# Kernel tuning notes

Hardware: AMD Instinct MI355X
Metric: run time of the kernel (lower is better)

Reference implementation:

```python
import jax, jax.numpy as jnp
import numpy as np

MIN_POS = 1e-6
EPS = 1e-20
B, S, F_IN, E, H = 2, 1024, 768, 768, 12
DH = E // H   # nnmf in_features per head (64)
FH = E // H   # nnmf out_features per head (hidden_features=embed_dim default)
N_NNMF_ITERS = 3
N_ALPHA_ITERS = 3


def l1norm(x, axis=-1):
    # F.normalize(x, p=1, dim=axis, eps=1e-20) for non-negative x
    return x / jnp.maximum(jnp.sum(jnp.abs(x), axis=axis, keepdims=True), EPS)


def setup_inputs() -> dict:
    key = jax.random.key(0)
    k = jax.random.split(key, 6)
    return {
        "x": jax.random.normal(k[0], (B, S, F_IN), jnp.float32),
        "embed_w": jax.random.normal(k[1], (E, F_IN), jnp.float32) * 0.02,
        "embed_b": jnp.zeros((E,), jnp.float32),
        "nnmf_w": jax.random.uniform(k[2], (FH, DH), jnp.float32),  # non-negative NMF dictionary
        "out_w": jax.random.normal(k[3], (F_IN, E), jnp.float32) * 0.02,
        "out_b": jnp.zeros((F_IN,), jnp.float32),
    }


def reference(x, embed_w, embed_b, nnmf_w, out_w, out_b):
    # normalize NMF weight rows (p=1 over in_features), as nnmf_layer.normalize_weights
    W = nnmf_w / jnp.maximum(jnp.sum(nnmf_w, axis=1, keepdims=True), EPS)  # [FH, DH]

    # embed + clamp positive, split heads
    xe = jnp.clip(x @ embed_w.T + embed_b, MIN_POS)            # [B,S,E]
    xe = xe.reshape(B, S, H, DH)                                # [B,S,H,DH]

    # NNMFDense: prepared_input = l1-normalized input (normalize_input_dim=-1)
    inp = l1norm(xe)                                            # [B,S,H,DH]
    h = l1norm(jnp.ones((B, S, H, FH), x.dtype))                # init hidden
    rec = inp
    for _ in range(N_NNMF_ITERS):
        rec = l1norm(jnp.clip(h @ W, MIN_POS))                  # reconstruction [B,S,H,DH]
        h = l1norm(jnp.clip(h * ((inp / rec) @ W.T), MIN_POS))  # multiplicative update

    # normalize_h (p=1, dim=-1)
    h = l1norm(h)                                               # [B,S,H,FH] -> 'bohf'

    # alpha dynamics fixed point
    alpha = jnp.ones((B, H, S, S), x.dtype)                     # 'bhoi'
    h_rec_input = rec * inp                                     # [B,S,H,DH]
    for _ in range(N_ALPHA_ITERS):
        h_mixed = jnp.einsum('bohf,bhoi->bihf', h, alpha)       # [B,S,H,FH]
        arec_inv = 1.0 / (h_mixed @ W + EPS)                    # _reconstruct -> [B,S,H,DH]
        alpha = alpha * jnp.einsum('bohf,bihf->bhoi', h_rec_input, arec_inv)

    out = jnp.einsum('bohf,bhoi->bihf', h, alpha)               # [B,S,H,FH]
    out = out.reshape(B, S, E)                                  # flatten heads
    return out @ out_w.T + out_b                                # out_project
```

## Files before the change

kernel.cpp:

```cpp
#include <hip/hip_runtime.h>

#define B_  2
#define S_  1024
#define FIN 768
#define E_  768
#define H_  12
#define DH  64

typedef unsigned int uint;
typedef unsigned short ushort;
typedef __attribute__((ext_vector_type(8))) short short8;
typedef __attribute__((ext_vector_type(4))) float floatx4;

__device__ __forceinline__ ushort f2bf(float f) {
    uint u = __float_as_uint(f);
    return (ushort)((u + 0x7fffu + ((u >> 16) & 1u)) >> 16);
}

__device__ __forceinline__ uint4 pack8(const ushort* p) {
    uint4 r;
    r.x = (uint)p[0] | ((uint)p[1] << 16);
    r.y = (uint)p[2] | ((uint)p[3] << 16);
    r.z = (uint)p[4] | ((uint)p[5] << 16);
    r.w = (uint)p[6] | ((uint)p[7] << 16);
    return r;
}

__device__ __forceinline__ void split8v(float4 a, float4 b, short8& hi, short8& lo) {
    float v[8] = {a.x, a.y, a.z, a.w, b.x, b.y, b.z, b.w};
    ushort h[8], l[8];
#pragma unroll
    for (int j = 0; j < 8; ++j) {
        h[j] = f2bf(v[j]);
        l[j] = f2bf(v[j] - __uint_as_float(((uint)h[j]) << 16));
    }
    uint4 H = pack8(h), L = pack8(l);
    hi = *(short8*)&H;
    lo = *(short8*)&L;
}

__global__ __launch_bounds__(256) void k_embed_prep(const float* __restrict__ xs,
                                                    const float* __restrict__ ew,
                                                    const float* __restrict__ eb,
                                                    const float* __restrict__ nw,
                                                    float* __restrict__ Wn,
                                                    float* __restrict__ WnT,
                                                    float* __restrict__ r1inv,
                                                    float* __restrict__ inp) {
    __shared__ __align__(16) unsigned char smem[28160];
    const int tid = threadIdx.x;
    const int bid = blockIdx.x;

    if (bid >= 768) {
        float* Wl = (float*)smem;
        const int f = tid >> 2, q = tid & 3;
        float v[16];
        float s = 0.f;
#pragma unroll
        for (int i = 0; i < 16; ++i) { v[i] = nw[f * 64 + q * 16 + i]; s += v[i]; }
        s += __shfl_xor(s, 1, 64);
        s += __shfl_xor(s, 2, 64);
        const float inv = 1.f / fmaxf(s, 1e-20f);
#pragma unroll
        for (int i = 0; i < 16; ++i) {
            float w = v[i] * inv;
            Wn[f * 64 + q * 16 + i] = w;
            WnT[(q * 16 + i) * 64 + f] = w;
            Wl[f * 65 + q * 16 + i] = w;
        }
        __syncthreads();
        if (tid < 64) {
            float cs = 0.f;
            for (int ff = 0; ff < 64; ++ff) cs += Wl[ff * 65 + tid];
            float t = fmaxf(cs * (1.f / 64.f), 1e-6f);
            float S = t;
#pragma unroll
            for (int m = 1; m < 64; m <<= 1) S += __shfl_xor(S, m, 64);
            S = fmaxf(S, 1e-20f);
            r1inv[tid] = S / t;
        }
        return;
    }

    const int head = bid % 12;
    const int tok0 = (bid / 12) * 32;
    ushort* As_hi = (ushort*)smem;
    ushort* As_lo = As_hi + 32 * 72;
    ushort* Bs_hi = As_lo + 32 * 72;
    ushort* Bs_lo = Bs_hi + 64 * 72;
    float*  RS    = (float*)(Bs_lo + 64 * 72);

    const int wv = tid >> 6, lane = tid & 63;
    const int mbase = (wv >> 1) * 16;
    const int nbase = (wv & 1) * 32;
    const int lm = lane & 15, lq = lane >> 4;

    floatx4 accA[2], accB[2];
    accA[0] = (floatx4)0.f; accA[1] = (floatx4)0.f;
    accB[0] = (floatx4)0.f; accB[1] = (floatx4)0.f;

    const int arow = tid >> 3, akc = (tid & 7) * 8;
    const int brow = tid >> 2, bkq = (tid & 3) * 16;
    const float* xrow = xs + (size_t)(tok0 + arow) * FIN + akc;
    const float* wrg  = ew + (size_t)(head * 64 + brow) * FIN + bkq;

    float4 pa[2], pb[4];
#pragma unroll
    for (int c = 0; c < 2; ++c) pa[c] = *(const float4*)(xrow + c * 4);
#pragma unroll
    for (int c = 0; c < 4; ++c) pb[c] = *(const float4*)(wrg + c * 4);

    for (int kb = 0; kb < FIN; kb += 64) {
        __syncthreads();
        {
            short8 Ah, Al, B0h, B0l, B1h, B1l;
            split8v(pa[0], pa[1], Ah, Al);
            split8v(pb[0], pb[1], B0h, B0l);
            split8v(pb[2], pb[3], B1h, B1l);
            const int aoff = arow * 72 + akc;
            *(short8*)&As_hi[aoff] = Ah;
            *(short8*)&As_lo[aoff] = Al;
            const int boff = brow * 72 + bkq;
            *(short8*)&Bs_hi[boff]     = B0h;
            *(short8*)&Bs_hi[boff + 8] = B1h;
            *(short8*)&Bs_lo[boff]     = B0l;
            *(short8*)&Bs_lo[boff + 8] = B1l;
        }
        __syncthreads();
        if (kb + 64 < FIN) {
#pragma unroll
            for (int c = 0; c < 2; ++c) pa[c] = *(const float4*)(xrow + kb + 64 + c * 4);
#pragma unroll
            for (int c = 0; c < 4; ++c) pb[c] = *(const float4*)(wrg + kb + 64 + c * 4);
        }
#pragma unroll
        for (int ch = 0; ch < 2; ++ch) {
            const int ko = ch * 32 + lq * 8;
            short8 ah = *(const short8*)&As_hi[(mbase + lm) * 72 + ko];
            short8 al = *(const short8*)&As_lo[(mbase + lm) * 72 + ko];
#pragma unroll
            for (int ti = 0; ti < 2; ++ti) {
                short8 bh = *(const short8*)&Bs_hi[(nbase + ti * 16 + lm) * 72 + ko];
                short8 bl = *(const short8*)&Bs_lo[(nbase + ti * 16 + lm) * 72 + ko];
                accA[ti] = __builtin_amdgcn_mfma_f32_16x16x32_bf16(ah, bh, accA[ti], 0, 0, 0);
                accB[ti] = __builtin_amdgcn_mfma_f32_16x16x32_bf16(al, bh, accB[ti], 0, 0, 0);
                accB[ti] = __builtin_amdgcn_mfma_f32_16x16x32_bf16(ah, bl, accB[ti], 0, 0, 0);
            }
        }
    }

    const float b0 = eb[head * 64 + nbase + lm];
    const float b1 = eb[head * 64 + nbase + 16 + lm];
    float xe[2][4];
    float rs[4];
#pragma unroll
    for (int r = 0; r < 4; ++r) {
        float e0 = fmaxf((accA[0][r] + accB[0][r]) + b0, 1e-6f);
        float e1 = fmaxf((accA[1][r] + accB[1][r]) + b1, 1e-6f);
        xe[0][r] = e0; xe[1][r] = e1;
        float p = e0 + e1;
        p += __shfl_xor(p, 1, 64);
        p += __shfl_xor(p, 2, 64);
        p += __shfl_xor(p, 4, 64);
        p += __shfl_xor(p, 8, 64);
        rs[r] = p;
    }
    if (lm == 0) {
#pragma unroll
        for (int r = 0; r < 4; ++r)
            RS[(wv & 1) * 32 + mbase + lq * 4 + r] = rs[r];
    }
    __syncthreads();
    const size_t obase = ((size_t)((tok0 >> 10) * 12 + head) * 1024 + (tok0 & 1023));
#pragma unroll
    for (int r = 0; r < 4; ++r) {
        const int m = mbase + lq * 4 + r;
        const float inv = 1.f / fmaxf(RS[m] + RS[32 + m], 1e-20f);
        float* op = inp + (obase + m) * 64;
        op[nbase + lm]      = xe[0][r] * inv;
        op[nbase + 16 + lm] = xe[1][r] * inv;
    }
}

__device__ __forceinline__ void mfma_matvec(const float srcC[4][4], float* T,
                                            int lm, int lq,
                                            const ushort* WH, const ushort* WL,
                                            floatx4 out[4]) {
    __builtin_amdgcn_wave_barrier();
#pragma unroll
    for (int nt = 0; nt < 4; ++nt)
#pragma unroll
        for (int r = 0; r < 4; ++r)
            T[(lq * 4 + r) * 68 + nt * 16 + lm] = srcC[nt][r];
    __builtin_amdgcn_wave_barrier();
    float4 a00 = *(const float4*)&T[lm * 68 + lq * 8];
    float4 a01 = *(const float4*)&T[lm * 68 + lq * 8 + 4];
    float4 a10 = *(const float4*)&T[lm * 68 + 32 + lq * 8];
    float4 a11 = *(const float4*)&T[lm * 68 + 32 + lq * 8 + 4];
    __builtin_amdgcn_wave_barrier();
    short8 A0h, A0l, A1h, A1l;
    split8v(a00, a01, A0h, A0l);
    split8v(a10, a11, A1h, A1l);
#pragma unroll
    for (int nt = 0; nt < 4; ++nt) {
        const int row = (nt * 16 + lm) * 72;
        short8 b0h = *(const short8*)&WH[row + lq * 8];
        short8 b0l = *(const short8*)&WL[row + lq * 8];
        short8 b1h = *(const short8*)&WH[row + 32 + lq * 8];
        short8 b1l = *(const short8*)&WL[row + 32 + lq * 8];
        floatx4 acc0 = (floatx4)0.f, acc1 = (floatx4)0.f;
        acc0 = __builtin_amdgcn_mfma_f32_16x16x32_bf16(A0h, b0h, acc0, 0, 0, 0);
        acc0 = __builtin_amdgcn_mfma_f32_16x16x32_bf16(A0l, b0h, acc0, 0, 0, 0);
        acc0 = __builtin_amdgcn_mfma_f32_16x16x32_bf16(A0h, b0l, acc0, 0, 0, 0);
        acc1 = __builtin_amdgcn_mfma_f32_16x16x32_bf16(A1h, b1h, acc1, 0, 0, 0);
        acc1 = __builtin_amdgcn_mfma_f32_16x16x32_bf16(A1l, b1h, acc1, 0, 0, 0);
        acc1 = __builtin_amdgcn_mfma_f32_16x16x32_bf16(A1h, b1l, acc1, 0, 0, 0);
        out[nt] = acc0 + acc1;
    }
}

__global__ __launch_bounds__(256) void k_nnmf(const float* __restrict__ inp,
                                              const float* __restrict__ Wn,
                                              const float* __restrict__ WnT,
                                              const float* __restrict__ r1inv,
                                              float* __restrict__ hout,
                                              float* __restrict__ hriout,
                                              float* __restrict__ mp0) {
    __shared__ ushort WtH[64 * 72], WtL[64 * 72];
    __shared__ ushort WwH[64 * 72], WwL[64 * 72];
    __shared__ float Tb[4][16 * 68];
    __shared__ float pbuf[256];
    const int tid = threadIdx.x, wv = tid >> 6, lane = tid & 63;
    const int lm = lane & 15, lq = lane >> 4;
    float* T = Tb[wv];
    const int rowbase = blockIdx.x * 64 + wv * 16;

    {
        const int row = tid >> 2, kq = (tid & 3) * 16;
        short8 h0, l0, h1, l1;
        split8v(*(const float4*)(WnT + row * 64 + kq), *(const float4*)(WnT + row * 64 + kq + 4), h0, l0);
        split8v(*(const float4*)(WnT + row * 64 + kq + 8), *(const float4*)(WnT + row * 64 + kq + 12), h1, l1);
        *(short8*)&WtH[row * 72 + kq] = h0; *(short8*)&WtH[row * 72 + kq + 8] = h1;
        *(short8*)&WtL[row * 72 + kq] = l0; *(short8*)&WtL[row * 72 + kq + 8] = l1;
        split8v(*(const float4*)(Wn + row * 64 + kq), *(const float4*)(Wn + row * 64 + kq + 4), h0, l0);
        split8v(*(const float4*)(Wn + row * 64 + kq + 8), *(const float4*)(Wn + row * 64 + kq + 12), h1, l1);
        *(short8*)&WwH[row * 72 + kq] = h0; *(short8*)&WwH[row * 72 + kq + 8] = h1;
        *(short8*)&WwL[row * 72 + kq] = l0; *(short8*)&WwL[row * 72 + kq + 8] = l1;
    }

    float inpC[4][4];
#pragma unroll
    for (int nt = 0; nt < 4; ++nt)
#pragma unroll
        for (int r = 0; r < 4; ++r)
            inpC[nt][r] = inp[(size_t)(rowbase + lq * 4 + r) * 64 + nt * 16 + lm];
    float r1c[4];
#pragma unroll
    for (int nt = 0; nt < 4; ++nt) r1c[nt] = r1inv[nt * 16 + lm];
    __syncthreads();

    float hC[4][4], recC[4][4];
    {
        float qC[4][4];
#pragma unroll
        for (int nt = 0; nt < 4; ++nt)
#pragma unroll
            for (int r = 0; r < 4; ++r) qC[nt][r] = inpC[nt][r] * r1c[nt];
        floatx4 u[4];
        mfma_matvec(qC, T, lm, lq, WwH, WwL, u);
#pragma unroll
        for (int nt = 0; nt < 4; ++nt)
#pragma unroll
            for (int r = 0; r < 4; ++r)
                hC[nt][r] = fmaxf(u[nt][r] * (1.f / 64.f), 1e-6f);
#pragma unroll
        for (int r = 0; r < 4; ++r) {
            float s = (hC[0][r] + hC[1][r]) + (hC[2][r] + hC[3][r]);
            s += __shfl_xor(s, 1, 64); s += __shfl_xor(s, 2, 64);
            s += __shfl_xor(s, 4, 64); s += __shfl_xor(s, 8, 64);
            const float inv = __builtin_amdgcn_rcpf(fmaxf(s, 1e-20f));
#pragma unroll
            for (int nt = 0; nt < 4; ++nt) hC[nt][r] *= inv;
        }
    }
#pragma unroll 1
    for (int it = 0; it < 2; ++it) {
        floatx4 t[4];
        mfma_matvec(hC, T, lm, lq, WtH, WtL, t);
        float tC[4][4], qC[4][4];
#pragma unroll
        for (int nt = 0; nt < 4; ++nt)
#pragma unroll
            for (int r = 0; r < 4; ++r) tC[nt][r] = fmaxf(t[nt][r], 1e-6f);
#pragma unroll
        for (int r = 0; r < 4; ++r) {
            float s = (tC[0][r] + tC[1][r]) + (tC[2][r] + tC[3][r]);
            s += __shfl_xor(s, 1, 64); s += __shfl_xor(s, 2, 64);
            s += __shfl_xor(s, 4, 64); s += __shfl_xor(s, 8, 64);
            s = fmaxf(s, 1e-20f);
            const float invS = __builtin_amdgcn_rcpf(s);
#pragma unroll
            for (int nt = 0; nt < 4; ++nt) {
                recC[nt][r] = tC[nt][r] * invS;
                qC[nt][r] = inpC[nt][r] * s * __builtin_amdgcn_rcpf(tC[nt][r]);
            }
        }
        floatx4 u[4];
        mfma_matvec(qC, T, lm, lq, WwH, WwL, u);
#pragma unroll
        for (int nt = 0; nt < 4; ++nt)
#pragma unroll
            for (int r = 0; r < 4; ++r)
                hC[nt][r] = fmaxf(hC[nt][r] * u[nt][r], 1e-6f);
#pragma unroll
        for (int r = 0; r < 4; ++r) {
            float s = (hC[0][r] + hC[1][r]) + (hC[2][r] + hC[3][r]);
            s += __shfl_xor(s, 1, 64); s += __shfl_xor(s, 2, 64);
            s += __shfl_xor(s, 4, 64); s += __shfl_xor(s, 8, 64);
            const float inv = __builtin_amdgcn_rcpf(fmaxf(s, 1e-20f));
#pragma unroll
            for (int nt = 0; nt < 4; ++nt) hC[nt][r] *= inv;
        }
    }
#pragma unroll
    for (int r = 0; r < 4; ++r) {
        float s = (hC[0][r] + hC[1][r]) + (hC[2][r] + hC[3][r]);
        s += __shfl_xor(s, 1, 64); s += __shfl_xor(s, 2, 64);
        s += __shfl_xor(s, 4, 64); s += __shfl_xor(s, 8, 64);
        const float inv = __builtin_amdgcn_rcpf(fmaxf(s, 1e-20f));
#pragma unroll
        for (int nt = 0; nt < 4; ++nt) hC[nt][r] *= inv;
    }

#pragma unroll
    for (int nt = 0; nt < 4; ++nt)
#pragma unroll
        for (int r = 0; r < 4; ++r) {
            const size_t o = (size_t)(rowbase + lq * 4 + r) * 64 + nt * 16 + lm;
            hout[o] = hC[nt][r];
            hriout[o] = recC[nt][r] * inpC[nt][r];
        }

    float hs[4];
#pragma unroll
    for (int nt = 0; nt < 4; ++nt) {
        float s = (hC[nt][0] + hC[nt][1]) + (hC[nt][2] + hC[nt][3]);
        s += __shfl_xor(s, 16, 64);
        s += __shfl_xor(s, 32, 64);
        hs[nt] = s;
    }
    pbuf[wv * 64 + lq * 16 + lm] = hs[lq];
    __syncthreads();
    if (tid < 64) {
        float tot = (pbuf[tid] + pbuf[64 + tid]) + (pbuf[128 + tid] + pbuf[192 + tid]);
        mp0[(size_t)blockIdx.x * 64 + tid] = tot;
    }
}

__global__ __launch_bounds__(256) void k_alpha_step(const float* __restrict__ hin,
                                                    const float* __restrict__ hri,
                                                    const float* __restrict__ Wn,
                                                    const float* __restrict__ mp_in,
                                                    float* __restrict__ mp_out,
                                                    float* __restrict__ c,
                                                    int it) {
    __shared__ float mred[4][64];
    __shared__ float mv[64];
    __shared__ float vv[64];
    __shared__ float cl[64];
    const int tid = threadIdx.x;
    const int bh = blockIdx.x >> 4;
    const int chunk = blockIdx.x & 15;
    const size_t rowbase = (size_t)bh * 1024 + chunk * 64;

    {
        int f = tid & 63, p = tid >> 6;
        float s = 0.f;
#pragma unroll
        for (int pp = 0; pp < 4; ++pp)
            s += mp_in[((size_t)bh * 16 + p * 4 + pp) * 64 + f];
        mred[p][f] = s;
    }
    __syncthreads();
    if (tid < 64)
        mv[tid] = (mred[0][tid] + mred[1][tid]) + (mred[2][tid] + mred[3][tid]);
    __syncthreads();
    {
        int d = tid & 63, qq = tid >> 6;
        float r = 0.f;
#pragma unroll
        for (int ff = 0; ff < 16; ++ff)
            r = fmaf(mv[qq * 16 + ff], Wn[(size_t)(qq * 16 + ff) * 64 + d], r);
        mred[qq][d] = r;
    }
    __syncthreads();
    if (tid < 64)
        vv[tid] = 1.f / (((mred[0][tid] + mred[1][tid]) + (mred[2][tid] + mred[3][tid])) + 1e-20f);
    __syncthreads();
    {
        int o = tid >> 2, dq = tid & 3;
        const float* rp = hri + (rowbase + o) * 64 + dq * 16;
        float dot = 0.f;
#pragma unroll
        for (int t4 = 0; t4 < 16; t4 += 4) {
            float4 r4 = *(const float4*)(rp + t4);
            dot = fmaf(r4.x, vv[dq * 16 + t4 + 0], dot);
            dot = fmaf(r4.y, vv[dq * 16 + t4 + 1], dot);
            dot = fmaf(r4.z, vv[dq * 16 + t4 + 2], dot);
            dot = fmaf(r4.w, vv[dq * 16 + t4 + 3], dot);
        }
        dot += __shfl_xor(dot, 1, 64);
        dot += __shfl_xor(dot, 2, 64);
        float cn = dot;
        if (it >= 2) cn *= c[rowbase + o];
        if (dq == 0) { c[rowbase + o] = cn; cl[o] = cn; }
    }
    __syncthreads();
    {
        const int f4 = (tid & 15) * 4, ogr = tid >> 4;
        float4 a = make_float4(0.f, 0.f, 0.f, 0.f);
#pragma unroll
        for (int oi = 0; oi < 4; ++oi) {
            int o = ogr * 4 + oi;
            float4 h4 = *(const float4*)(hin + (rowbase + o) * 64 + f4);
            float cv = cl[o];
            a.x = fmaf(h4.x, cv, a.x); a.y = fmaf(h4.y, cv, a.y);
            a.z = fmaf(h4.z, cv, a.z); a.w = fmaf(h4.w, cv, a.w);
        }
        a.x += __shfl_xor(a.x, 16, 64); a.y += __shfl_xor(a.y, 16, 64);
        a.z += __shfl_xor(a.z, 16, 64); a.w += __shfl_xor(a.w, 16, 64);
        a.x += __shfl_xor(a.x, 32, 64); a.y += __shfl_xor(a.y, 32, 64);
        a.z += __shfl_xor(a.z, 32, 64); a.w += __shfl_xor(a.w, 32, 64);
        const int w = tid >> 6;
        if ((tid & 63) < 16) *(float4*)&mred[w][(tid & 15) * 4] = a;
    }
    __syncthreads();
    if (tid < 64) {
        float s = (mred[0][tid] + mred[1][tid]) + (mred[2][tid] + mred[3][tid]);
        mp_out[((size_t)bh * 16 + chunk) * 64 + tid] = s;
    }
}

__global__ __launch_bounds__(256) void k_projbcast(const float* __restrict__ mp3,
                                                   const float* __restrict__ ow,
                                                   const float* __restrict__ ob,
                                                   float* __restrict__ out) {
    __shared__ float Ml[768];
    __shared__ float ps[4][64];
    __shared__ float yseg[64];
    const int tid = threadIdx.x;
    const int b = blockIdx.x / 192;
    const int rem = blockIdx.x - b * 192;
    const int jt = rem >> 4, rg = rem & 15;
    for (int i = tid; i < 768; i += 256) {
        const int hh = i >> 6, f = i & 63;
        const float* src = mp3 + ((size_t)(b * 12 + hh) * 16) * 64 + f;
        float s = 0.f;
#pragma unroll
        for (int cc = 0; cc < 16; ++cc) s += src[cc * 64];
        Ml[i] = s;
    }
    __syncthreads();
    const int jj = tid & 63, part = tid >> 6;
    const int j = jt * 64 + jj;
    const float* row = ow + (size_t)j * 768 + part * 192;
    float acc = 0.f;
    for (int t = 0; t < 192; t += 4) {
        float4 w4 = *(const float4*)(row + t);
        acc = fmaf(w4.x, Ml[part * 192 + t + 0], acc);
        acc = fmaf(w4.y, Ml[part * 192 + t + 1], acc);
        acc = fmaf(w4.z, Ml[part * 192 + t + 2], acc);
        acc = fmaf(w4.w, Ml[part * 192 + t + 3], acc);
    }
    ps[part][jj] = acc;
    __syncthreads();
    if (tid < 64)
        yseg[tid] = ps[0][tid] + ps[1][tid] + ps[2][tid] + ps[3][tid] + ob[jt * 64 + tid];
    __syncthreads();
    const int r0 = tid >> 2, c4 = (tid & 3) * 16;
    float4 v4[4];
#pragma unroll
    for (int q = 0; q < 4; ++q) v4[q] = *(const float4*)&yseg[c4 + q * 4];
    float* dst = out + ((size_t)(b * 1024 + rg * 64 + r0)) * 768 + jt * 64 + c4;
#pragma unroll
    for (int q = 0; q < 4; ++q) *(float4*)(dst + q * 4) = v4[q];
}

extern "C" void kernel_launch(void* const* d_in, const int* in_sizes, int n_in,
                              void* d_out, int out_size, void* d_ws, size_t ws_size,
                              hipStream_t stream) {
    const float* xs = (const float*)d_in[0];
    const float* ew = (const float*)d_in[1];
    const float* eb = (const float*)d_in[2];
    const float* nw = (const float*)d_in[3];
    const float* ow = (const float*)d_in[4];
    const float* ob = (const float*)d_in[5];
    float* out = (float*)d_out;

    float* ws    = (float*)d_ws;
    float* inp   = ws;
    float* h     = ws + 1572864;
    float* hri   = ws + 3145728;
    float* Wn    = ws + 4718592;
    float* WnT   = ws + 4722688;
    float* r1inv = ws + 4726784;
    float* mp0   = ws + 4727040;
    float* mp1   = ws + 4751616;
    float* mp2   = ws + 4776192;
    float* c     = ws + 4800768;

    k_embed_prep<<<769, 256, 0, stream>>>(xs, ew, eb, nw, Wn, WnT, r1inv, inp);
    k_nnmf<<<384, 256, 0, stream>>>(inp, Wn, WnT, r1inv, h, hri, mp0);
    k_alpha_step<<<384, 256, 0, stream>>>(h, hri, Wn, mp0, mp1, c, 1);
    k_alpha_step<<<384, 256, 0, stream>>>(h, hri, Wn, mp1, mp2, c, 2);
    k_alpha_step<<<384, 256, 0, stream>>>(h, hri, Wn, mp2, mp1, c, 3);
    k_projbcast<<<384, 256, 0, stream>>>(mp1, ow, ob, out);
}
```

Measured before the change: 133.0 us.

## Pre-split embed inputs and NMF weights into bf16 hi/lo in a conversion kernel

Adds a k_conv kernel that converts x and embed_w once into bf16 hi/lo arrays, normalizes the NMF dictionary, and writes both orientations of it as pre-split bf16 fragments. The embed GEMM then loads ready-made bf16 pairs instead of re-splitting fp32 tiles in every block, and k_nnmf copies the pre-split fragments instead of converting W per block. The aim is to remove redundant conversion work: in the old code each x tile is split once per head (12 times) and each weight tile once per token block. The cost is an extra launch plus a round trip of roughly 2x the x and embed_w data through global memory.

```diff
diff --git a/kernel.cpp b/kernel.cpp
--- a/kernel.cpp
+++ b/kernel.cpp
@@ -39,48 +39,102 @@
     lo = *(short8*)&L;
 }
 
-__global__ __launch_bounds__(256) void k_embed_prep(const float* __restrict__ xs,
-                                                    const float* __restrict__ ew,
-                                                    const float* __restrict__ eb,
-                                                    const float* __restrict__ nw,
-                                                    float* __restrict__ Wn,
-                                                    float* __restrict__ WnT,
-                                                    float* __restrict__ r1inv,
-                                                    float* __restrict__ inp) {
+__global__ __launch_bounds__(256) void k_conv(const float* __restrict__ xs,
+                                              const float* __restrict__ ew,
+                                              const float* __restrict__ nw,
+                                              ushort* __restrict__ xsH,
+                                              ushort* __restrict__ xsL,
+                                              ushort* __restrict__ ewH,
+                                              ushort* __restrict__ ewL,
+                                              float* __restrict__ Wn,
+                                              float* __restrict__ r1inv,
+                                              ushort* __restrict__ Wfrag) {
+    __shared__ float Wl[64 * 65];
+    const int tid = threadIdx.x, bid = blockIdx.x;
+
+    if (bid < 768) {
+        const size_t i = ((size_t)bid * 256 + tid) * 8;
+        short8 hi, lo;
+        split8v(*(const float4*)(xs + i), *(const float4*)(xs + i + 4), hi, lo);
+        *(short8*)(xsH + i) = hi;
+        *(short8*)(xsL + i) = lo;
+        return;
+    }
+    if (bid < 1056) {
+        const size_t i = ((size_t)(bid - 768) * 256 + tid) * 8;
+        short8 hi, lo;
+        split8v(*(const float4*)(ew + i), *(const float4*)(ew + i + 4), hi, lo);
+        *(short8*)(ewH + i) = hi;
+        *(short8*)(ewL + i) = lo;
+        return;
+    }
+
+    const int f = tid >> 2, q = tid & 3;
+    float v[16];
+    float s = 0.f;
+#pragma unroll
+    for (int i = 0; i < 16; ++i) { v[i] = nw[f * 64 + q * 16 + i]; s += v[i]; }
+    s += __shfl_xor(s, 1, 64);
+    s += __shfl_xor(s, 2, 64);
+    const float inv = 1.f / fmaxf(s, 1e-20f);
+    float w[16];
+#pragma unroll
+    for (int i = 0; i < 16; ++i) {
+        w[i] = v[i] * inv;
+        Wn[f * 64 + q * 16 + i] = w[i];
+        Wl[f * 65 + q * 16 + i] = w[i];
+    }
+    __syncthreads();
+    if (tid < 64) {
+        float cs = 0.f;
+        for (int ff = 0; ff < 64; ++ff) cs += Wl[ff * 65 + tid];
+        float t = fmaxf(cs * (1.f / 64.f), 1e-6f);
+        float S = t;
+#pragma unroll
+        for (int m = 1; m < 64; m <<= 1) S += __shfl_xor(S, m, 64);
+        S = fmaxf(S, 1e-20f);
+        r1inv[tid] = S / t;
+    }
+    {
+        short8 h0, l0, h1, l1;
+        split8v(make_float4(w[0], w[1], w[2], w[3]),
+                make_float4(w[4], w[5], w[6], w[7]), h0, l0);
+        split8v(make_float4(w[8], w[9], w[10], w[11]),
+                make_float4(w[12], w[13], w[14], w[15]), h1, l1);
+        ushort* WwH = Wfrag + 2 * 4096;
+        ushort* WwL = Wfrag + 3 * 4096;
+        *(short8*)(WwH + f * 64 + q * 16) = h0;
+        *(short8*)(WwH + f * 64 + q * 16 + 8) = h1;
+        *(short8*)(WwL + f * 64 + q * 16) = l0;
+        *(short8*)(WwL + f * 64 + q * 16 + 8) = l1;
+    }
+    {
+        float t[16];
+#pragma unroll
+        for (int i = 0; i < 16; ++i) t[i] = Wl[(q * 16 + i) * 65 + f];
+        short8 h0, l0, h1, l1;
+        split8v(make_float4(t[0], t[1], t[2], t[3]),
+                make_float4(t[4], t[5], t[6], t[7]), h0, l0);
+        split8v(make_float4(t[8], t[9], t[10], t[11]),
+                make_float4(t[12], t[13], t[14], t[15]), h1, l1);
+        ushort* WtH = Wfrag;
+        ushort* WtL = Wfrag + 4096;
+        *(short8*)(WtH + f * 64 + q * 16) = h0;
+        *(short8*)(WtH + f * 64 + q * 16 + 8) = h1;
+        *(short8*)(WtL + f * 64 + q * 16) = l0;
+        *(short8*)(WtL + f * 64 + q * 16 + 8) = l1;
+    }
+}
+
+__global__ __launch_bounds__(256) void k_embed(const ushort* __restrict__ xsH,
+                                               const ushort* __restrict__ xsL,
+                                               const ushort* __restrict__ ewH,
+                                               const ushort* __restrict__ ewL,
+                                               const float* __restrict__ eb,
+                                               float* __restrict__ inp) {
     __shared__ __align__(16) unsigned char smem[28160];
     const int tid = threadIdx.x;
     const int bid = blockIdx.x;
-
-    if (bid >= 768) {
-        float* Wl = (float*)smem;
-        const int f = tid >> 2, q = tid & 3;
-        float v[16];
-        float s = 0.f;
-#pragma unroll
-        for (int i = 0; i < 16; ++i) { v[i] = nw[f * 64 + q * 16 + i]; s += v[i]; }
-        s += __shfl_xor(s, 1, 64);
-        s += __shfl_xor(s, 2, 64);
-        const float inv = 1.f / fmaxf(s, 1e-20f);
-#pragma unroll
-        for (int i = 0; i < 16; ++i) {
-            float w = v[i] * inv;
-            Wn[f * 64 + q * 16 + i] = w;
-            WnT[(q * 16 + i) * 64 + f] = w;
-            Wl[f * 65 + q * 16 + i] = w;
-        }
-        __syncthreads();
-        if (tid < 64) {
-            float cs = 0.f;
-            for (int ff = 0; ff < 64; ++ff) cs += Wl[ff * 65 + tid];
-            float t = fmaxf(cs * (1.f / 64.f), 1e-6f);
-            float S = t;
-#pragma unroll
-            for (int m = 1; m < 64; m <<= 1) S += __shfl_xor(S, m, 64);
-            S = fmaxf(S, 1e-20f);
-            r1inv[tid] = S / t;
-        }
-        return;
-    }
 
     const int head = bid % 12;
     const int tok0 = (bid / 12) * 32;
@@ -101,37 +155,40 @@
 
     const int arow = tid >> 3, akc = (tid & 7) * 8;
     const int brow = tid >> 2, bkq = (tid & 3) * 16;
-    const float* xrow = xs + (size_t)(tok0 + arow) * FIN + akc;
-    const float* wrg  = ew + (size_t)(head * 64 + brow) * FIN + bkq;
-
-    float4 pa[2], pb[4];
-#pragma unroll
-    for (int c = 0; c < 2; ++c) pa[c] = *(const float4*)(xrow + c * 4);
-#pragma unroll
-    for (int c = 0; c < 4; ++c) pb[c] = *(const float4*)(wrg + c * 4);
+    const ushort* xh = xsH + (size_t)(tok0 + arow) * FIN + akc;
+    const ushort* xl = xsL + (size_t)(tok0 + arow) * FIN + akc;
+    const ushort* wh = ewH + (size_t)(head * 64 + brow) * FIN + bkq;
+    const ushort* wl = ewL + (size_t)(head * 64 + brow) * FIN + bkq;
+
+    short8 pah, pal, pbh0, pbh1, pbl0, pbl1;
+    pah  = *(const short8*)(xh);
+    pal  = *(const short8*)(xl);
+    pbh0 = *(const short8*)(wh);
+    pbh1 = *(const short8*)(wh + 8);
+    pbl0 = *(const short8*)(wl);
+    pbl1 = *(const short8*)(wl + 8);
 
     for (int kb = 0; kb < FIN; kb += 64) {
         __syncthreads();
         {
-            short8 Ah, Al, B0h, B0l, B1h, B1l;
-            split8v(pa[0], pa[1], Ah, Al);
-            split8v(pb[0], pb[1], B0h, B0l);
-            split8v(pb[2], pb[3], B1h, B1l);
             const int aoff = arow * 72 + akc;
-            *(short8*)&As_hi[aoff] = Ah;
-            *(short8*)&As_lo[aoff] = Al;
+            *(short8*)&As_hi[aoff] = pah;
+            *(short8*)&As_lo[aoff] = pal;
             const int boff = brow * 72 + bkq;
-            *(short8*)&Bs_hi[boff]     = B0h;
-            *(short8*)&Bs_hi[boff + 8] = B1h;
-            *(short8*)&Bs_lo[boff]     = B0l;
-            *(short8*)&Bs_lo[boff + 8] = B1l;
+            *(short8*)&Bs_hi[boff]     = pbh0;
+            *(short8*)&Bs_hi[boff + 8] = pbh1;
+            *(short8*)&Bs_lo[boff]     = pbl0;
+            *(short8*)&Bs_lo[boff + 8] = pbl1;
         }
         __syncthreads();
         if (kb + 64 < FIN) {
-#pragma unroll
-            for (int c = 0; c < 2; ++c) pa[c] = *(const float4*)(xrow + kb + 64 + c * 4);
-#pragma unroll
-            for (int c = 0; c < 4; ++c) pb[c] = *(const float4*)(wrg + kb + 64 + c * 4);
+            const int ko = kb + 64;
+            pah  = *(const short8*)(xh + ko);
+            pal  = *(const short8*)(xl + ko);
+            pbh0 = *(const short8*)(wh + ko);
+            pbh1 = *(const short8*)(wh + ko + 8);
+            pbl0 = *(const short8*)(wl + ko);
+            pbl1 = *(const short8*)(wl + ko + 8);
         }
 #pragma unroll
         for (int ch = 0; ch < 2; ++ch) {
@@ -220,8 +277,7 @@
 }
 
 __global__ __launch_bounds__(256) void k_nnmf(const float* __restrict__ inp,
-                                              const float* __restrict__ Wn,
-                                              const float* __restrict__ WnT,
+                                              const ushort* __restrict__ Wfrag,
                                               const float* __restrict__ r1inv,
                                               float* __restrict__ hout,
                                               float* __restrict__ hriout,
@@ -237,15 +293,15 @@
 
     {
         const int row = tid >> 2, kq = (tid & 3) * 16;
-        short8 h0, l0, h1, l1;
-        split8v(*(const float4*)(WnT + row * 64 + kq), *(const float4*)(WnT + row * 64 + kq + 4), h0, l0);
-        split8v(*(const float4*)(WnT + row * 64 + kq + 8), *(const float4*)(WnT + row * 64 + kq + 12), h1, l1);
-        *(short8*)&WtH[row * 72 + kq] = h0; *(short8*)&WtH[row * 72 + kq + 8] = h1;
-        *(short8*)&WtL[row * 72 + kq] = l0; *(short8*)&WtL[row * 72 + kq + 8] = l1;
-        split8v(*(const float4*)(Wn + row * 64 + kq), *(const float4*)(Wn + row * 64 + kq + 4), h0, l0);
-        split8v(*(const float4*)(Wn + row * 64 + kq + 8), *(const float4*)(Wn + row * 64 + kq + 12), h1, l1);
-        *(short8*)&WwH[row * 72 + kq] = h0; *(short8*)&WwH[row * 72 + kq + 8] = h1;
-        *(short8*)&WwL[row * 72 + kq] = l0; *(short8*)&WwL[row * 72 + kq + 8] = l1;
+        const int g = row * 64 + kq, l = row * 72 + kq;
+        *(short8*)&WtH[l]     = *(const short8*)(Wfrag + g);
+        *(short8*)&WtH[l + 8] = *(const short8*)(Wfrag + g + 8);
+        *(short8*)&WtL[l]     = *(const short8*)(Wfrag + 4096 + g);
+        *(short8*)&WtL[l + 8] = *(const short8*)(Wfrag + 4096 + g + 8);
+        *(short8*)&WwH[l]     = *(const short8*)(Wfrag + 8192 + g);
+        *(short8*)&WwH[l + 8] = *(const short8*)(Wfrag + 8192 + g + 8);
+        *(short8*)&WwL[l]     = *(const short8*)(Wfrag + 12288 + g);
+        *(short8*)&WwL[l + 8] = *(const short8*)(Wfrag + 12288 + g + 8);
     }
 
     float inpC[4][4];
@@ -502,15 +558,20 @@
     float* h     = ws + 1572864;
     float* hri   = ws + 3145728;
     float* Wn    = ws + 4718592;
-    float* WnT   = ws + 4722688;
-    float* r1inv = ws + 4726784;
-    float* mp0   = ws + 4727040;
-    float* mp1   = ws + 4751616;
-    float* mp2   = ws + 4776192;
-    float* c     = ws + 4800768;
-
-    k_embed_prep<<<769, 256, 0, stream>>>(xs, ew, eb, nw, Wn, WnT, r1inv, inp);
-    k_nnmf<<<384, 256, 0, stream>>>(inp, Wn, WnT, r1inv, h, hri, mp0);
+    float* r1inv = ws + 4722688;
+    float* mp0   = ws + 4722944;
+    float* mp1   = ws + 4747520;
+    float* mp2   = ws + 4772096;
+    float* c     = ws + 4796672;
+    ushort* xsH  = (ushort*)(ws + 4821248);
+    ushort* xsL  = (ushort*)(ws + 5607680);
+    ushort* ewH  = (ushort*)(ws + 6394112);
+    ushort* ewL  = (ushort*)(ws + 6689024);
+    ushort* Wfrag= (ushort*)(ws + 6983936);
+
+    k_conv<<<1057, 256, 0, stream>>>(xs, ew, nw, xsH, xsL, ewH, ewL, Wn, r1inv, Wfrag);
+    k_embed<<<768, 256, 0, stream>>>(xsH, xsL, ewH, ewL, eb, inp);
+    k_nnmf<<<384, 256, 0, stream>>>(inp, Wfrag, r1inv, h, hri, mp0);
     k_alpha_step<<<384, 256, 0, stream>>>(h, hri, Wn, mp0, mp1, c, 1);
     k_alpha_step<<<384, 256, 0, stream>>>(h, hri, Wn, mp1, mp2, c, 2);
     k_alpha_step<<<384, 256, 0, stream>>>(h, hri, Wn, mp2, mp1, c, 3);
```

After: 131.5 us. Within noise of the previous version (-1.2%).
